# Kernel optimization log

Hardware: AMD Instinct MI355X
Metric: run time of the kernel (lower is better)

The kernel has to match this reference:

```python
import jax, jax.numpy as jnp
import numpy as np

B, N, F, H, L = 8, 512, 32, 64, 2

def setup_inputs() -> dict:
    key = jax.random.key(0)
    ks = jax.random.split(key, 16)
    s = lambda fan_in: 1.0 / np.sqrt(fan_in)
    return {
        "x": jax.random.normal(ks[0], (B, N, F), dtype=jnp.float32),
        # node encoder: Linear(F, H), stored as [in, out]
        "W_enc": jax.random.uniform(ks[1], (F, H), minval=-s(F), maxval=s(F)),
        "b_enc": jax.random.uniform(ks[2], (H,), minval=-s(F), maxval=s(F)),
        # edge MLP: Linear(2H, H) then Linear(H, 1)
        "W_e1": jax.random.uniform(ks[3], (2 * H, H), minval=-s(2 * H), maxval=s(2 * H)),
        "b_e1": jax.random.uniform(ks[4], (H,), minval=-s(2 * H), maxval=s(2 * H)),
        "W_e2": jax.random.uniform(ks[5], (H,), minval=-s(H), maxval=s(H)),
        "b_e2": jax.random.uniform(ks[6], (), minval=-s(H), maxval=s(H)),
        # per-layer message Linear(H, H)
        "W_msg": jax.random.uniform(ks[7], (L, H, H), minval=-s(H), maxval=s(H)),
        "b_msg": jax.random.uniform(ks[8], (L, H), minval=-s(H), maxval=s(H)),
        # per-layer GRUCell(H, H): gates ordered [r, z, n], stored as [in, 3H]
        "W_ih": jax.random.uniform(ks[9], (L, H, 3 * H), minval=-s(H), maxval=s(H)),
        "b_ih": jax.random.uniform(ks[10], (L, 3 * H), minval=-s(H), maxval=s(H)),
        "W_hh": jax.random.uniform(ks[11], (L, H, 3 * H), minval=-s(H), maxval=s(H)),
        "b_hh": jax.random.uniform(ks[12], (L, 3 * H), minval=-s(H), maxval=s(H)),
        # output Linear(H, 1)
        "W_out": jax.random.uniform(ks[13], (H, 1), minval=-s(H), maxval=s(H)),
        "b_out": jax.random.uniform(ks[14], (1,), minval=-s(H), maxval=s(H)),
    }

def reference(x, W_enc, b_enc, W_e1, b_e1, W_e2, b_e2, W_msg, b_msg,
              W_ih, b_ih, W_hh, b_hh, W_out, b_out):
    # Node encoding (dropout is eval-mode identity)
    h = jax.nn.relu(x @ W_enc + b_enc)  # [B, N, H]

    # Edge MLP on pairwise concat [h_i, h_j]: split W_e1 so we never build the 2H concat
    Wa, Wb = W_e1[:H], W_e1[H:]
    zi = h @ Wa                           # contribution of h_i, [B, N, H]
    zj = h @ Wb                           # contribution of h_j, [B, N, H]
    e = jax.nn.relu(zi[:, :, None, :] + zj[:, None, :, :] + b_e1)  # [B, N, N, H]
    logits = jnp.einsum('bijh,h->bij', e, W_e2) + b_e2             # [B, N, N]

    eye = jnp.eye(logits.shape[-1], dtype=bool)
    logits = jnp.where(eye[None], -jnp.inf, logits)
    adj = jax.nn.softmax(logits, axis=-1)
    adj = jnp.nan_to_num(adj, nan=0.0, posinf=0.0, neginf=0.0)

    for l in range(L):
        m = jnp.einsum('bij,bjh->bih', adj, h)             # message aggregation
        m = jax.nn.relu(m @ W_msg[l] + b_msg[l])
        # GRUCell update (gates [r, z, n])
        gi = m @ W_ih[l] + b_ih[l]
        gh = h @ W_hh[l] + b_hh[l]
        ir, iz, inn = jnp.split(gi, 3, axis=-1)
        hr, hz, hn = jnp.split(gh, 3, axis=-1)
        r = jax.nn.sigmoid(ir + hr)
        z = jax.nn.sigmoid(iz + hz)
        n = jnp.tanh(inn + r * hn)
        h = (1.0 - z) * n + z * h

    graph_emb = jnp.mean(h, axis=1)       # [B, H]
    return graph_emb @ W_out + b_out      # [B, 1]
```

## Files before the change

### kernel.cpp

```cpp
#include <hip/hip_runtime.h>
#include <math.h>

#define BB 8
#define NN 512
#define FF 32
#define HH 64
#define NEG_BIG (-1.0e30f)

__device__ __forceinline__ float lane_bcast(float v, int l) {
    return __int_as_float(__builtin_amdgcn_readlane(__float_as_int(v), l));
}

__global__ __launch_bounds__(256) void encode_kernel(
    const float* __restrict__ x, const float* __restrict__ W_enc,
    const float* __restrict__ b_enc, const float* __restrict__ W_e1,
    const float* __restrict__ b_e1,
    float* __restrict__ h, float* __restrict__ zi, float* __restrict__ zjT2)
{
    const int t = threadIdx.x;
    const int hh = t & 63;
    const int qu = __builtin_amdgcn_readfirstlane(t >> 6);
    const int gR = blockIdx.x * 4 + qu;

    const float xv = x[gR * FF + (hh & 31)];
    float acc = b_enc[hh];
#pragma unroll 8
    for (int k = 0; k < FF; ++k)
        acc = fmaf(lane_bcast(xv, k), W_enc[k * HH + hh], acc);
    const float hval = fmaxf(acc, 0.f);
    h[gR * HH + hh] = hval;

    float z1 = b_e1[hh], z2 = 0.f;
#pragma unroll 8
    for (int k = 0; k < HH; ++k) {
        const float hk = lane_bcast(hval, k);
        z1 = fmaf(hk, W_e1[k * HH + hh], z1);
        z2 = fmaf(hk, W_e1[(HH + k) * HH + hh], z2);
    }
    zi[gR * HH + hh] = z1;
    const int b = gR >> 9, n = gR & (NN - 1);
    zjT2[(((size_t)b * 32 + (hh >> 1)) * NN + n) * 2 + (hh & 1)] = z2;
}

template <int MODE>
__global__ __launch_bounds__(512, 4) void adjlayer_kernel(
    const float* __restrict__ zi, const float* __restrict__ zjT2,
    const float* __restrict__ We2, const float* __restrict__ be2,
    float* __restrict__ adjw, const float* __restrict__ h_in,
    const float* __restrict__ Wmsg, const float* __restrict__ bmsg,
    const float* __restrict__ Wih, const float* __restrict__ bih,
    const float* __restrict__ Whh, const float* __restrict__ bhh,
    float* __restrict__ h_out, float* __restrict__ partial)
{
    const int b  = blockIdx.x >> 6;
    const int i0 = (blockIdx.x & 63) << 3;
    const int t  = threadIdx.x;
    const int tj = t & 63;
    const int w  = __builtin_amdgcn_readfirstlane(t >> 6);
    const int gR0 = b * NN + i0;
    const int j   = 64 * w + tj;

    __shared__ float smem[6336];
    __shared__ float mml[8][66];
    __shared__ float hol[8][66];
    __shared__ float redm[8][8], reds[8][8];
#define RED(p, r, c)        smem[(((p) * 8) + (r)) * 66 + (c)]
#define GP(h2, k2, r, g, c) smem[(((((h2) * 2 + (k2)) * 8 + (r)) * 3 + (g)) * 66) + (c)]

    hol[w][tj] = h_in[(size_t)(gR0 + w) * HH + tj];

    float va[8];
    if (MODE == 0) {
        const float2* zi2 = (const float2*)(zi + (size_t)gR0 * HH);
        const float2* we2 = (const float2*)We2;
        const float2* zt2 = (const float2*)zjT2 + (size_t)b * 32 * NN + j;

        float2 a2[8];
#pragma unroll
        for (int r = 0; r < 8; ++r) a2[r] = make_float2(0.f, 0.f);
#pragma unroll 8
        for (int k2 = 0; k2 < 32; ++k2) {
            const float2 z = zt2[(size_t)k2 * NN];
            const float2 wk = we2[k2];
#pragma unroll
            for (int r = 0; r < 8; ++r) {
                const float2 zv = zi2[r * 32 + k2];
                a2[r].x = fmaf(fmaxf(zv.x + z.x, 0.f), wk.x, a2[r].x);
                a2[r].y = fmaf(fmaxf(zv.y + z.y, 0.f), wk.y, a2[r].y);
            }
        }
        const float bias2 = be2[0];
        float acc[8];
#pragma unroll
        for (int r = 0; r < 8; ++r) {
            acc[r] = a2[r].x + a2[r].y + bias2;
            if (j == i0 + r) acc[r] = NEG_BIG;
        }

#pragma unroll
        for (int r = 0; r < 8; ++r) {
            float m = acc[r];
#pragma unroll
            for (int off = 32; off >= 1; off >>= 1)
                m = fmaxf(m, __shfl_xor(m, off));
            if (tj == 0) redm[w][r] = m;
        }
        __syncthreads();
        float M[8];
#pragma unroll
        for (int r = 0; r < 8; ++r) {
            float m = redm[0][r];
#pragma unroll
            for (int p = 1; p < 8; ++p) m = fmaxf(m, redm[p][r]);
            M[r] = m;
        }
#pragma unroll
        for (int r = 0; r < 8; ++r) {
            va[r] = __expf(acc[r] - M[r]);
            float s = va[r];
#pragma unroll
            for (int off = 32; off >= 1; off >>= 1) s += __shfl_xor(s, off);
            if (tj == 0) reds[w][r] = s;
        }
        __syncthreads();
#pragma unroll
        for (int r = 0; r < 8; ++r) {
            float s = reds[0][r];
#pragma unroll
            for (int p = 1; p < 8; ++p) s += reds[p][r];
            va[r] *= 1.0f / s;
            adjw[(size_t)(gR0 + r) * NN + j] = va[r];
        }
    } else {
#pragma unroll
        for (int r = 0; r < 8; ++r)
            va[r] = adjw[(size_t)(gR0 + r) * NN + j];
    }

    {
        const float* hq = h_in + ((size_t)b * NN + 64 * w) * HH + tj;
        float mac[8] = {0.f, 0.f, 0.f, 0.f, 0.f, 0.f, 0.f, 0.f};
#pragma unroll 4
        for (int jj = 0; jj < 64; ++jj) {
            const float hv = hq[(size_t)jj * HH];
#pragma unroll
            for (int r = 0; r < 8; ++r)
                mac[r] = fmaf(lane_bcast(va[r], jj), hv, mac[r]);
        }
#pragma unroll
        for (int r = 0; r < 8; ++r) RED(w, r, tj) = mac[r];
    }
    __syncthreads();

    {
        float m = RED(0, w, tj);
#pragma unroll
        for (int p = 1; p < 8; ++p) m += RED(p, w, tj);
        float mmv = bmsg[tj];
#pragma unroll 8
        for (int k = 0; k < HH; ++k)
            mmv = fmaf(lane_bcast(m, k), Wmsg[k * HH + tj], mmv);
        mml[w][tj] = fmaxf(mmv, 0.f);
    }
    __syncthreads();

    {
        const int half = w >> 2, kh = (w >> 1) & 1, rq = w & 1;
        const float* Wg = half ? Whh : Wih;
        const float* bg = half ? bhh : bih;
        float sreg[4];
#pragma unroll
        for (int r = 0; r < 4; ++r)
            sreg[r] = half ? hol[rq * 4 + r][tj] : mml[rq * 4 + r][tj];
        float g0[4], g1[4], g2[4];
#pragma unroll
        for (int r = 0; r < 4; ++r) {
            g0[r] = kh ? 0.f : bg[tj];
            g1[r] = kh ? 0.f : bg[64 + tj];
            g2[r] = kh ? 0.f : bg[128 + tj];
        }
        const int k0 = kh * 32;
#pragma unroll 4
        for (int kk = 0; kk < 32; ++kk) {
            const float* wk = Wg + (size_t)(k0 + kk) * 192;
            const float w0 = wk[tj], w1 = wk[64 + tj], w2 = wk[128 + tj];
#pragma unroll
            for (int r = 0; r < 4; ++r) {
                const float s = lane_bcast(sreg[r], k0 + kk);
                g0[r] = fmaf(s, w0, g0[r]);
                g1[r] = fmaf(s, w1, g1[r]);
                g2[r] = fmaf(s, w2, g2[r]);
            }
        }
#pragma unroll
        for (int r = 0; r < 4; ++r) {
            GP(half, kh, rq * 4 + r, 0, tj) = g0[r];
            GP(half, kh, rq * 4 + r, 1, tj) = g1[r];
            GP(half, kh, rq * 4 + r, 2, tj) = g2[r];
        }
    }
    __syncthreads();

    float hnew;
    {
        const float ir  = GP(0, 0, w, 0, tj) + GP(0, 1, w, 0, tj);
        const float iz  = GP(0, 0, w, 1, tj) + GP(0, 1, w, 1, tj);
        const float inn = GP(0, 0, w, 2, tj) + GP(0, 1, w, 2, tj);
        const float hr  = GP(1, 0, w, 0, tj) + GP(1, 1, w, 0, tj);
        const float hz  = GP(1, 0, w, 1, tj) + GP(1, 1, w, 1, tj);
        const float hn  = GP(1, 0, w, 2, tj) + GP(1, 1, w, 2, tj);
        const float rg = 1.f / (1.f + __expf(-(ir + hr)));
        const float zg = 1.f / (1.f + __expf(-(iz + hz)));
        const float ng = tanhf(inn + rg * hn);
        hnew = (1.f - zg) * ng + zg * hol[w][tj];
        h_out[(size_t)(gR0 + w) * HH + tj] = hnew;
    }

    if (MODE == 1) {
        __syncthreads();
        mml[w][tj] = hnew;
        __syncthreads();
        if (w == 0) {
            float s = 0.f;
#pragma unroll
            for (int r = 0; r < 8; ++r) s += mml[r][tj];
            partial[blockIdx.x * 64 + tj] = s;
        }
    }
#undef RED
#undef GP
}

__global__ __launch_bounds__(64) void readout_kernel(
    const float* __restrict__ partial, const float* __restrict__ W_out,
    const float* __restrict__ b_out, float* __restrict__ out)
{
    const int b = blockIdx.x;
    const int hh = threadIdx.x;
    float s = 0.f;
#pragma unroll 8
    for (int c = 0; c < 64; ++c)
        s += partial[(b * 64 + c) * 64 + hh];
    float v = s * (1.0f / NN) * W_out[hh];
#pragma unroll
    for (int off = 32; off >= 1; off >>= 1) v += __shfl_xor(v, off);
    if (hh == 0) out[b] = v + b_out[0];
}

extern "C" void kernel_launch(void* const* d_in, const int* in_sizes, int n_in,
                              void* d_out, int out_size, void* d_ws, size_t ws_size,
                              hipStream_t stream)
{
    const float* x     = (const float*)d_in[0];
    const float* W_enc = (const float*)d_in[1];
    const float* b_enc = (const float*)d_in[2];
    const float* W_e1  = (const float*)d_in[3];
    const float* b_e1  = (const float*)d_in[4];
    const float* W_e2  = (const float*)d_in[5];
    const float* b_e2  = (const float*)d_in[6];
    const float* W_msg = (const float*)d_in[7];
    const float* b_msg = (const float*)d_in[8];
    const float* W_ih  = (const float*)d_in[9];
    const float* b_ih  = (const float*)d_in[10];
    const float* W_hh  = (const float*)d_in[11];
    const float* b_hh  = (const float*)d_in[12];
    const float* W_out = (const float*)d_in[13];
    const float* b_out = (const float*)d_in[14];
    float* out = (float*)d_out;

    float* ws   = (float*)d_ws;
    float* h0   = ws;
    float* h1   = h0 + BB * NN * HH;
    float* zi   = h1 + BB * NN * HH;
    float* zjT2 = zi + BB * NN * HH;
    float* prt  = zjT2 + BB * NN * HH;
    float* adjw = prt + 512 * 64;

    encode_kernel<<<BB * NN / 4, 256, 0, stream>>>(
        x, W_enc, b_enc, W_e1, b_e1, h0, zi, zjT2);

    adjlayer_kernel<0><<<BB * (NN / 8), 512, 0, stream>>>(
        zi, zjT2, W_e2, b_e2, adjw, h0,
        W_msg, b_msg, W_ih, b_ih, W_hh, b_hh, h1, nullptr);
    adjlayer_kernel<1><<<BB * (NN / 8), 512, 0, stream>>>(
        zi, zjT2, W_e2, b_e2, adjw, h1,
        W_msg + HH * HH, b_msg + HH,
        W_ih + HH * 3 * HH, b_ih + 3 * HH, W_hh + HH * 3 * HH, b_hh + 3 * HH,
        h0, prt);

    readout_kernel<<<BB, 64, 0, stream>>>(prt, W_out, b_out, out);
}
```

Before: 74.07 us.

## Halve rows per block to double grid size and read adjacency directly in layer two

Each adjacency/layer block now handles 4 query rows instead of 8, so the grid doubles to 1024 blocks and the launch bound allows 8 blocks per CU. This targets poor occupancy and load balance on a GPU with many CUs. In the second layer, adjacency values are now read straight from global memory in the aggregation loop instead of being loaded into registers and broadcast across lanes. The cost is that zjT2 and h_in get reloaded by twice as many blocks, half the waves sit idle in the message and GRU stages, and the readout has twice as many partials to sum.

```diff
diff --git a/kernel.cpp b/kernel.cpp
--- a/kernel.cpp
+++ b/kernel.cpp
@@ -43,62 +43,63 @@
 }
 
 template <int MODE>
-__global__ __launch_bounds__(512, 4) void adjlayer_kernel(
+__global__ __launch_bounds__(512, 8) void adjlayer_kernel(
     const float* __restrict__ zi, const float* __restrict__ zjT2,
     const float* __restrict__ We2, const float* __restrict__ be2,
-    float* __restrict__ adjw, const float* __restrict__ h_in,
+    float* __restrict__ adjw, const float* __restrict__ adjr,
+    const float* __restrict__ h_in,
     const float* __restrict__ Wmsg, const float* __restrict__ bmsg,
     const float* __restrict__ Wih, const float* __restrict__ bih,
     const float* __restrict__ Whh, const float* __restrict__ bhh,
     float* __restrict__ h_out, float* __restrict__ partial)
 {
-    const int b  = blockIdx.x >> 6;
-    const int i0 = (blockIdx.x & 63) << 3;
+    const int b  = blockIdx.x >> 7;
+    const int i0 = (blockIdx.x & 127) << 2;
     const int t  = threadIdx.x;
     const int tj = t & 63;
     const int w  = __builtin_amdgcn_readfirstlane(t >> 6);
     const int gR0 = b * NN + i0;
     const int j   = 64 * w + tj;
 
-    __shared__ float smem[6336];
-    __shared__ float mml[8][66];
-    __shared__ float hol[8][66];
-    __shared__ float redm[8][8], reds[8][8];
-#define RED(p, r, c)        smem[(((p) * 8) + (r)) * 66 + (c)]
-#define GP(h2, k2, r, g, c) smem[(((((h2) * 2 + (k2)) * 8 + (r)) * 3 + (g)) * 66) + (c)]
-
-    hol[w][tj] = h_in[(size_t)(gR0 + w) * HH + tj];
-
-    float va[8];
+    __shared__ float smem[3168];
+    __shared__ float mml[4][66];
+    __shared__ float hol[4][66];
+    __shared__ float redm[8][4], reds[8][4];
+#define RED(p, r, c)        smem[(((p) * 4) + (r)) * 66 + (c)]
+#define GP(h2, k2, r, g, c) smem[(((((h2) * 2 + (k2)) * 4 + (r)) * 3 + (g)) * 66) + (c)]
+
+    if (w < 4) hol[w][tj] = h_in[(size_t)(gR0 + w) * HH + tj];
+
+    float va[4];
     if (MODE == 0) {
         const float2* zi2 = (const float2*)(zi + (size_t)gR0 * HH);
         const float2* we2 = (const float2*)We2;
         const float2* zt2 = (const float2*)zjT2 + (size_t)b * 32 * NN + j;
 
-        float2 a2[8];
-#pragma unroll
-        for (int r = 0; r < 8; ++r) a2[r] = make_float2(0.f, 0.f);
+        float2 a2[4];
+#pragma unroll
+        for (int r = 0; r < 4; ++r) a2[r] = make_float2(0.f, 0.f);
 #pragma unroll 8
         for (int k2 = 0; k2 < 32; ++k2) {
             const float2 z = zt2[(size_t)k2 * NN];
             const float2 wk = we2[k2];
 #pragma unroll
-            for (int r = 0; r < 8; ++r) {
+            for (int r = 0; r < 4; ++r) {
                 const float2 zv = zi2[r * 32 + k2];
                 a2[r].x = fmaf(fmaxf(zv.x + z.x, 0.f), wk.x, a2[r].x);
                 a2[r].y = fmaf(fmaxf(zv.y + z.y, 0.f), wk.y, a2[r].y);
             }
         }
         const float bias2 = be2[0];
-        float acc[8];
-#pragma unroll
-        for (int r = 0; r < 8; ++r) {
+        float acc[4];
+#pragma unroll
+        for (int r = 0; r < 4; ++r) {
             acc[r] = a2[r].x + a2[r].y + bias2;
             if (j == i0 + r) acc[r] = NEG_BIG;
         }
 
 #pragma unroll
-        for (int r = 0; r < 8; ++r) {
+        for (int r = 0; r < 4; ++r) {
             float m = acc[r];
 #pragma unroll
             for (int off = 32; off >= 1; off >>= 1)
@@ -106,16 +107,16 @@
             if (tj == 0) redm[w][r] = m;
         }
         __syncthreads();
-        float M[8];
-#pragma unroll
-        for (int r = 0; r < 8; ++r) {
+        float M[4];
+#pragma unroll
+        for (int r = 0; r < 4; ++r) {
             float m = redm[0][r];
 #pragma unroll
             for (int p = 1; p < 8; ++p) m = fmaxf(m, redm[p][r]);
             M[r] = m;
         }
 #pragma unroll
-        for (int r = 0; r < 8; ++r) {
+        for (int r = 0; r < 4; ++r) {
             va[r] = __expf(acc[r] - M[r]);
             float s = va[r];
 #pragma unroll
@@ -124,35 +125,46 @@
         }
         __syncthreads();
 #pragma unroll
-        for (int r = 0; r < 8; ++r) {
+        for (int r = 0; r < 4; ++r) {
             float s = reds[0][r];
 #pragma unroll
             for (int p = 1; p < 8; ++p) s += reds[p][r];
             va[r] *= 1.0f / s;
             adjw[(size_t)(gR0 + r) * NN + j] = va[r];
         }
-    } else {
-#pragma unroll
-        for (int r = 0; r < 8; ++r)
-            va[r] = adjw[(size_t)(gR0 + r) * NN + j];
     }
 
     {
         const float* hq = h_in + ((size_t)b * NN + 64 * w) * HH + tj;
-        float mac[8] = {0.f, 0.f, 0.f, 0.f, 0.f, 0.f, 0.f, 0.f};
+        float mac[4] = {0.f, 0.f, 0.f, 0.f};
+        if (MODE == 0) {
 #pragma unroll 4
-        for (int jj = 0; jj < 64; ++jj) {
-            const float hv = hq[(size_t)jj * HH];
-#pragma unroll
-            for (int r = 0; r < 8; ++r)
-                mac[r] = fmaf(lane_bcast(va[r], jj), hv, mac[r]);
-        }
-#pragma unroll
-        for (int r = 0; r < 8; ++r) RED(w, r, tj) = mac[r];
+            for (int jj = 0; jj < 64; ++jj) {
+                const float hv = hq[(size_t)jj * HH];
+#pragma unroll
+                for (int r = 0; r < 4; ++r)
+                    mac[r] = fmaf(lane_bcast(va[r], jj), hv, mac[r]);
+            }
+        } else {
+            const float* a0 = adjr + (size_t)(gR0 + 0) * NN + 64 * w;
+            const float* a1 = adjr + (size_t)(gR0 + 1) * NN + 64 * w;
+            const float* a2 = adjr + (size_t)(gR0 + 2) * NN + 64 * w;
+            const float* a3 = adjr + (size_t)(gR0 + 3) * NN + 64 * w;
+#pragma unroll 8
+            for (int jj = 0; jj < 64; ++jj) {
+                const float hv = hq[(size_t)jj * HH];
+                mac[0] = fmaf(a0[jj], hv, mac[0]);
+                mac[1] = fmaf(a1[jj], hv, mac[1]);
+                mac[2] = fmaf(a2[jj], hv, mac[2]);
+                mac[3] = fmaf(a3[jj], hv, mac[3]);
+            }
+        }
+#pragma unroll
+        for (int r = 0; r < 4; ++r) RED(w, r, tj) = mac[r];
     }
     __syncthreads();
 
-    {
+    if (w < 4) {
         float m = RED(0, w, tj);
 #pragma unroll
         for (int p = 1; p < 8; ++p) m += RED(p, w, tj);
@@ -168,13 +180,13 @@
         const int half = w >> 2, kh = (w >> 1) & 1, rq = w & 1;
         const float* Wg = half ? Whh : Wih;
         const float* bg = half ? bhh : bih;
-        float sreg[4];
-#pragma unroll
-        for (int r = 0; r < 4; ++r)
-            sreg[r] = half ? hol[rq * 4 + r][tj] : mml[rq * 4 + r][tj];
-        float g0[4], g1[4], g2[4];
-#pragma unroll
-        for (int r = 0; r < 4; ++r) {
+        float sreg[2];
+#pragma unroll
+        for (int r = 0; r < 2; ++r)
+            sreg[r] = half ? hol[rq * 2 + r][tj] : mml[rq * 2 + r][tj];
+        float g0[2], g1[2], g2[2];
+#pragma unroll
+        for (int r = 0; r < 2; ++r) {
             g0[r] = kh ? 0.f : bg[tj];
             g1[r] = kh ? 0.f : bg[64 + tj];
             g2[r] = kh ? 0.f : bg[128 + tj];
@@ -185,7 +197,7 @@
             const float* wk = Wg + (size_t)(k0 + kk) * 192;
             const float w0 = wk[tj], w1 = wk[64 + tj], w2 = wk[128 + tj];
 #pragma unroll
-            for (int r = 0; r < 4; ++r) {
+            for (int r = 0; r < 2; ++r) {
                 const float s = lane_bcast(sreg[r], k0 + kk);
                 g0[r] = fmaf(s, w0, g0[r]);
                 g1[r] = fmaf(s, w1, g1[r]);
@@ -193,16 +205,16 @@
             }
         }
 #pragma unroll
-        for (int r = 0; r < 4; ++r) {
-            GP(half, kh, rq * 4 + r, 0, tj) = g0[r];
-            GP(half, kh, rq * 4 + r, 1, tj) = g1[r];
-            GP(half, kh, rq * 4 + r, 2, tj) = g2[r];
+        for (int r = 0; r < 2; ++r) {
+            GP(half, kh, rq * 2 + r, 0, tj) = g0[r];
+            GP(half, kh, rq * 2 + r, 1, tj) = g1[r];
+            GP(half, kh, rq * 2 + r, 2, tj) = g2[r];
         }
     }
     __syncthreads();
 
-    float hnew;
-    {
+    float hnew = 0.f;
+    if (w < 4) {
         const float ir  = GP(0, 0, w, 0, tj) + GP(0, 1, w, 0, tj);
         const float iz  = GP(0, 0, w, 1, tj) + GP(0, 1, w, 1, tj);
         const float inn = GP(0, 0, w, 2, tj) + GP(0, 1, w, 2, tj);
@@ -218,13 +230,11 @@
 
     if (MODE == 1) {
         __syncthreads();
-        mml[w][tj] = hnew;
+        if (w < 4) mml[w][tj] = hnew;
         __syncthreads();
         if (w == 0) {
-            float s = 0.f;
-#pragma unroll
-            for (int r = 0; r < 8; ++r) s += mml[r][tj];
-            partial[blockIdx.x * 64 + tj] = s;
+            partial[blockIdx.x * 64 + tj] =
+                mml[0][tj] + mml[1][tj] + mml[2][tj] + mml[3][tj];
         }
     }
 #undef RED
@@ -239,8 +249,8 @@
     const int hh = threadIdx.x;
     float s = 0.f;
 #pragma unroll 8
-    for (int c = 0; c < 64; ++c)
-        s += partial[(b * 64 + c) * 64 + hh];
+    for (int c = 0; c < 128; ++c)
+        s += partial[(b * 128 + c) * 64 + hh];
     float v = s * (1.0f / NN) * W_out[hh];
 #pragma unroll
     for (int off = 32; off >= 1; off >>= 1) v += __shfl_xor(v, off);
@@ -274,16 +284,16 @@
     float* zi   = h1 + BB * NN * HH;
     float* zjT2 = zi + BB * NN * HH;
     float* prt  = zjT2 + BB * NN * HH;
-    float* adjw = prt + 512 * 64;
+    float* adjw = prt + 1024 * 64;
 
     encode_kernel<<<BB * NN / 4, 256, 0, stream>>>(
         x, W_enc, b_enc, W_e1, b_e1, h0, zi, zjT2);
 
-    adjlayer_kernel<0><<<BB * (NN / 8), 512, 0, stream>>>(
-        zi, zjT2, W_e2, b_e2, adjw, h0,
+    adjlayer_kernel<0><<<BB * (NN / 4), 512, 0, stream>>>(
+        zi, zjT2, W_e2, b_e2, adjw, adjw, h0,
         W_msg, b_msg, W_ih, b_ih, W_hh, b_hh, h1, nullptr);
-    adjlayer_kernel<1><<<BB * (NN / 8), 512, 0, stream>>>(
-        zi, zjT2, W_e2, b_e2, adjw, h1,
+    adjlayer_kernel<1><<<BB * (NN / 4), 512, 0, stream>>>(
+        zi, zjT2, W_e2, b_e2, adjw, adjw, h1,
         W_msg + HH * HH, b_msg + HH,
         W_ih + HH * 3 * HH, b_ih + 3 * HH, W_hh + HH * 3 * HH, b_hh + 3 * HH,
         h0, prt);
```

Result: no change. 72.78 us (-1.7%).
